# Kernel tuning notes

Hardware: AMD Instinct MI355X
Metric: run time of the kernel (lower is better)

## Reference

```python
import jax, jax.numpy as jnp
import numpy as np

N = 4096          # n_nodes
D = 7             # ligand_dim
H = 8             # dim_h
CUTOFF = 3.6      # bond_cutoff


def _linear_init(key, fan_in, fan_out):
    k1, k2 = jax.random.split(key)
    s = 1.0 / np.sqrt(fan_in)
    w = jax.random.uniform(k1, (fan_in, fan_out), minval=-s, maxval=s, dtype=jnp.float32)
    b = jax.random.uniform(k2, (fan_out,), minval=-s, maxval=s, dtype=jnp.float32)
    return w, b


def setup_inputs() -> dict:
    key = jax.random.key(0)
    ks = jax.random.split(key, 6)
    w1, b1 = _linear_init(ks[0], D, H)          # model layer 1
    w2, b2 = _linear_init(ks[1], H, H)          # model layer 2
    w3, b3 = _linear_init(ks[2], H, D + 16)     # model layer 3 (feats | keys | queries)
    we, be = _linear_init(ks[3], 2 * D, H)      # encoder
    wd, bd = _linear_init(ks[4], H, D)          # decoder
    x = jax.random.normal(ks[5], (N, D), dtype=jnp.float32)
    return dict(x=x, w1=w1, b1=b1, w2=w2, b2=b2, w3=w3, b3=b3,
                we=we, be=be, wd=wd, bd=bd)


def reference(x, w1, b1, w2, b2, w3, b3, we, be, wd, bd):
    # --- build_graph on detached x: L1 distance over first 3 coords ---
    # (sum(sqrt(abs(a-b)**2)) == sum(abs(a-b)))
    pos = jax.lax.stop_gradient(x[:, :3])
    dist = jnp.zeros((N, N), dtype=x.dtype)
    for d in range(3):  # loop over 3 coords to avoid an [N,N,3] intermediate
        dist = dist + jnp.abs(pos[:, d][:, None] - pos[None, :, d])
    A = (dist <= CUTOFF).astype(x.dtype)  # [N, N] adjacency
    # temp_input[-1] is never reset in the original kk loop, so node kk's
    # attention list is the cumulative multiset of neighbors of nodes 0..kk.
    C = jnp.cumsum(A, axis=0)             # [N, N] multiplicity of node l in kk's list

    # --- tiny MLP (shared per node) ---
    h = jnp.arctan(x @ w1 + b1)
    h = jnp.arctan(h @ w2 + b2)
    m = h @ w3 + b3                       # [N, D+16]
    feats = m[:, :D]                      # aggregated message payload
    keys_ = m[:, D:D + 8]                 # temp[:, -16:-8]
    queries = m[:, D + 8:]                # temp[:, -8:]

    # attention score of a list element depends only on its source node:
    # score = dot(queries[mm], keys[mm])
    s = jnp.sum(queries * keys_, axis=1)  # [N]

    # softmax over the cumulative multiset: weight of node l in row kk is
    # C[kk,l] * exp(s_l) / sum_l' C[kk,l'] * exp(s_l')   (stable via masked max)
    mask = C > 0
    smax = jnp.max(jnp.where(mask, s[None, :], -jnp.inf), axis=1)    # [N]
    w = C * jnp.where(mask, jnp.exp(s[None, :] - smax[:, None]), 0.0)  # [N, N]
    agg = (w @ feats) / jnp.sum(w, axis=1, keepdims=True)            # [N, D]

    # --- encode / decode ---
    codes = jnp.arctan(jnp.concatenate([x, agg], axis=1) @ we + be)  # [N, H]
    new_graph = codes @ wd + bd                                      # [N, D]
    return new_graph
```

## Files before the change

### kernel.cpp

```cpp
#include <hip/hip_runtime.h>
#include <math.h>

#define NN 4096
#define DD 7
#define HH 8
#define CUT 3.6f
#define JSPLIT 16
#define JCH 256
#define NRT 16
#define TPB 512


__global__ __launch_bounds__(TPB) void k_pair(
    const float* __restrict__ x,
    const float* __restrict__ w1, const float* __restrict__ b1,
    const float* __restrict__ w2, const float* __restrict__ b2,
    const float* __restrict__ w3, const float* __restrict__ b3,
    float* __restrict__ part, float* __restrict__ bsum)
{
    __shared__ float4 tile[JCH * 3];
    __shared__ float  red1[64][8];
    __shared__ float  red2[8][8];
    const int xb = blockIdx.x;
    const int y  = blockIdx.y;
    const int t  = threadIdx.x;

    if (t < JCH) {
        const int jg = y * JCH + t;
        float xi[DD];
#pragma unroll
        for (int i = 0; i < DD; ++i) xi[i] = x[jg * DD + i];

        float h1[HH];
#pragma unroll
        for (int o = 0; o < HH; ++o) {
            float a = b1[o];
#pragma unroll
            for (int i = 0; i < DD; ++i) a = fmaf(xi[i], w1[i * HH + o], a);
            h1[o] = atanf(a);
        }
        float h2[HH];
#pragma unroll
        for (int o = 0; o < HH; ++o) {
            float a = b2[o];
#pragma unroll
            for (int i = 0; i < HH; ++i) a = fmaf(h1[i], w2[i * HH + o], a);
            h2[o] = atanf(a);
        }
        float m[23];
#pragma unroll
        for (int c = 0; c < 23; ++c) {
            float a = b3[c];
#pragma unroll
            for (int i = 0; i < HH; ++i) a = fmaf(h2[i], w3[i * 23 + c], a);
            m[c] = a;
        }
        float s = 0.f;
#pragma unroll
        for (int k = 0; k < 8; ++k) s = fmaf(m[15 + k], m[7 + k], s);
        const float e = expf(s);

        tile[t * 3 + 0] = make_float4(xi[0], xi[1], xi[2], e);
        tile[t * 3 + 1] = make_float4(e * m[0], e * m[1], e * m[2], e * m[3]);
        tile[t * 3 + 2] = make_float4(e * m[4], e * m[5], e * m[6], 0.f);
    }
    __syncthreads();

    const int jl   = t & 7;
    const int grp  = t >> 3;
    const int row0 = xb * 256 + grp * 4;

    float px[4][3];
#pragma unroll
    for (int rr = 0; rr < 4; ++rr) {
        px[rr][0] = x[(row0 + rr) * DD + 0];
        px[rr][1] = x[(row0 + rr) * DD + 1];
        px[rr][2] = x[(row0 + rr) * DD + 2];
    }

    float acc[4][8];
#pragma unroll
    for (int rr = 0; rr < 4; ++rr)
#pragma unroll
        for (int ch = 0; ch < 8; ++ch) acc[rr][ch] = 0.f;

#pragma unroll 4
    for (int k = 0; k < JCH / 8; ++k) {
        const int jj = k * 8 + jl;
        float4 a = tile[jj * 3 + 0];
        float4 b = tile[jj * 3 + 1];
        float4 c = tile[jj * 3 + 2];
#pragma unroll
        for (int rr = 0; rr < 4; ++rr) {
            float dist = fabsf(px[rr][0] - a.x) + fabsf(px[rr][1] - a.y)
                       + fabsf(px[rr][2] - a.z);
            float msel = (dist <= CUT) ? 1.0f : 0.0f;
            acc[rr][0] = fmaf(msel, b.x, acc[rr][0]);
            acc[rr][1] = fmaf(msel, b.y, acc[rr][1]);
            acc[rr][2] = fmaf(msel, b.z, acc[rr][2]);
            acc[rr][3] = fmaf(msel, b.w, acc[rr][3]);
            acc[rr][4] = fmaf(msel, c.x, acc[rr][4]);
            acc[rr][5] = fmaf(msel, c.y, acc[rr][5]);
            acc[rr][6] = fmaf(msel, c.z, acc[rr][6]);
            acc[rr][7] = fmaf(msel, a.w, acc[rr][7]);
        }
    }

#pragma unroll
    for (int rr = 0; rr < 4; ++rr)
#pragma unroll
        for (int ch = 0; ch < 8; ++ch) {
            float v = acc[rr][ch];
            v += __shfl_xor(v, 4, 8);
            v += __shfl_xor(v, 2, 8);
            v += __shfl_xor(v, 1, 8);
            acc[rr][ch] = v;
        }

    if (jl == 0) {
#pragma unroll
        for (int ch = 0; ch < 8; ++ch) {
            float4* pp = (float4*)(part + (size_t)(y * 8 + ch) * NN + row0);
            *pp = make_float4(acc[0][ch], acc[1][ch], acc[2][ch], acc[3][ch]);
            red1[grp][ch] = ((acc[0][ch] + acc[1][ch]) + (acc[2][ch] + acc[3][ch]));
        }
    }
    __syncthreads();
    if (t < 64) {
        const int ch = t & 7, seg = t >> 3;
        float s = 0.f;
#pragma unroll
        for (int g = 0; g < 8; ++g) s += red1[seg * 8 + g][ch];
        red2[seg][ch] = s;
    }
    __syncthreads();
    if (t < 8) {
        float s = 0.f;
#pragma unroll
        for (int seg = 0; seg < 8; ++seg) s += red2[seg][t];
        bsum[xb * 128 + y * 8 + t] = s;
    }
}

__global__ __launch_bounds__(256) void k_scanfinal(
    const float* __restrict__ x, const float* __restrict__ part,
    const float* __restrict__ bsum,
    const float* __restrict__ we, const float* __restrict__ be,
    const float* __restrict__ wd, const float* __restrict__ bd,
    float* __restrict__ out)
{
    const int b = blockIdx.x;
    const int t = threadIdx.x;

    __shared__ float red[256];
    __shared__ float basech[8];
    __shared__ float wtot[4][8];

    {
        float p = 0.f;
        for (int i = t; i < b * 128; i += 256) p += bsum[i];
        red[t] = p;
    }
    __syncthreads();
    if (t < 8) {
        float s = 0.f;
#pragma unroll
        for (int q = 0; q < 32; ++q) s += red[t + 8 * q];
        basech[t] = s;
    }

    const int k = b * 256 + t;
    float T[8];
#pragma unroll
    for (int ch = 0; ch < 8; ++ch) {
        float v = 0.f;
#pragma unroll
        for (int y = 0; y < JSPLIT; ++y)
            v += part[(size_t)(y * 8 + ch) * NN + k];
        T[ch] = v;
    }

    const int lane = t & 63, wv = t >> 6;
    float sc[8];
#pragma unroll
    for (int ch = 0; ch < 8; ++ch) {
        float v = T[ch];
#pragma unroll
        for (int off = 1; off < 64; off <<= 1) {
            float o = __shfl_up(v, off, 64);
            if (lane >= off) v += o;
        }
        if (lane == 63) wtot[wv][ch] = v;
        sc[ch] = v;
    }
    __syncthreads();

    float pref[8];
#pragma unroll
    for (int ch = 0; ch < 8; ++ch) {
        float woff = basech[ch];
#pragma unroll
        for (int w = 0; w < 4; ++w) if (w < wv) woff += wtot[w][ch];
        pref[ch] = woff + sc[ch];
    }

    float v[14];
#pragma unroll
    for (int i = 0; i < DD; ++i) v[i] = x[k * DD + i];
    const float den = pref[7];
#pragma unroll
    for (int d = 0; d < DD; ++d) v[DD + d] = pref[d] / den;

    float codes[HH];
#pragma unroll
    for (int o = 0; o < HH; ++o) {
        float a = be[o];
#pragma unroll
        for (int i = 0; i < 14; ++i) a = fmaf(v[i], we[i * HH + o], a);
        codes[o] = atanf(a);
    }
#pragma unroll
    for (int d = 0; d < DD; ++d) {
        float a = bd[d];
#pragma unroll
        for (int o = 0; o < HH; ++o) a = fmaf(codes[o], wd[o * DD + d], a);
        out[k * DD + d] = a;
    }
}

extern "C" void kernel_launch(void* const* d_in, const int* in_sizes, int n_in,
                              void* d_out, int out_size, void* d_ws, size_t ws_size,
                              hipStream_t stream)
{
    const float* x  = (const float*)d_in[0];
    const float* w1 = (const float*)d_in[1];
    const float* b1 = (const float*)d_in[2];
    const float* w2 = (const float*)d_in[3];
    const float* b2 = (const float*)d_in[4];
    const float* w3 = (const float*)d_in[5];
    const float* b3 = (const float*)d_in[6];
    const float* we = (const float*)d_in[7];
    const float* be = (const float*)d_in[8];
    const float* wd = (const float*)d_in[9];
    const float* bd = (const float*)d_in[10];
    float* out = (float*)d_out;

    float* part = (float*)d_ws;
    float* bsum = part + (size_t)JSPLIT * 8 * NN;

    k_pair     <<<dim3(NRT, JSPLIT), TPB, 0, stream>>>(x, w1, b1, w2, b2, w3, b3,
                                                       part, bsum);
    k_scanfinal<<<NRT, 256, 0, stream>>>(x, part, bsum, we, be, wd, bd, out);
}
```

Before: 26.22 us.

## Fuse pair and scan kernels using a global atomic grid barrier

Merges the pairwise accumulation kernel and the scan/finalize kernel into one launch. All 256 blocks bump a global counter when done, and the first 16 blocks spin on it before running the prefix scan and the encoder/decoder. This removes the gap between dependent kernel launches, but adds a memset launch to reset the counter, busy-waiting, and the assumption that every block is resident at once. It also places a __syncthreads inside a branch only half the threads take.

```diff
diff --git a/kernel.cpp b/kernel.cpp
--- a/kernel.cpp
+++ b/kernel.cpp
@@ -9,21 +9,30 @@
 #define JCH 256
 #define NRT 16
 #define TPB 512
-
-
-__global__ __launch_bounds__(TPB) void k_pair(
+#define NBLK (NRT * JSPLIT)
+
+
+__global__ __launch_bounds__(TPB) void k_fused(
     const float* __restrict__ x,
     const float* __restrict__ w1, const float* __restrict__ b1,
     const float* __restrict__ w2, const float* __restrict__ b2,
     const float* __restrict__ w3, const float* __restrict__ b3,
-    float* __restrict__ part, float* __restrict__ bsum)
+    const float* __restrict__ we, const float* __restrict__ be,
+    const float* __restrict__ wd, const float* __restrict__ bd,
+    float* __restrict__ part, float* __restrict__ bsum,
+    int* __restrict__ sem, float* __restrict__ out)
 {
     __shared__ float4 tile[JCH * 3];
     __shared__ float  red1[64][8];
     __shared__ float  red2[8][8];
-    const int xb = blockIdx.x;
-    const int y  = blockIdx.y;
-    const int t  = threadIdx.x;
+    __shared__ float  red[256];
+    __shared__ float  basech[8];
+    __shared__ float  wtot[4][8];
+
+    const int blk = blockIdx.x;
+    const int xb  = blk >> 4;
+    const int y   = blk & 15;
+    const int t   = threadIdx.x;
 
     if (t < JCH) {
         const int jg = y * JCH + t;
@@ -140,23 +149,22 @@
         for (int seg = 0; seg < 8; ++seg) s += red2[seg][t];
         bsum[xb * 128 + y * 8 + t] = s;
     }
-}
-
-__global__ __launch_bounds__(256) void k_scanfinal(
-    const float* __restrict__ x, const float* __restrict__ part,
-    const float* __restrict__ bsum,
-    const float* __restrict__ we, const float* __restrict__ be,
-    const float* __restrict__ wd, const float* __restrict__ bd,
-    float* __restrict__ out)
-{
-    const int b = blockIdx.x;
-    const int t = threadIdx.x;
-
-    __shared__ float red[256];
-    __shared__ float basech[8];
-    __shared__ float wtot[4][8];
-
-    {
+
+    __threadfence();
+    __syncthreads();
+    if (t == 0)
+        __hip_atomic_fetch_add(sem, 1, __ATOMIC_RELEASE, __HIP_MEMORY_SCOPE_AGENT);
+    if (blk >= 16) return;
+
+    if (t == 0) {
+        while (__hip_atomic_load(sem, __ATOMIC_ACQUIRE, __HIP_MEMORY_SCOPE_AGENT)
+               < NBLK) {}
+    }
+    __syncthreads();
+    __threadfence();
+
+    const int b = blk;
+    if (t < 256) {
         float p = 0.f;
         for (int i = t; i < b * 128; i += 256) p += bsum[i];
         red[t] = p;
@@ -168,63 +176,66 @@
         for (int q = 0; q < 32; ++q) s += red[t + 8 * q];
         basech[t] = s;
     }
-
-    const int k = b * 256 + t;
-    float T[8];
-#pragma unroll
-    for (int ch = 0; ch < 8; ++ch) {
-        float v = 0.f;
-#pragma unroll
-        for (int y = 0; y < JSPLIT; ++y)
-            v += part[(size_t)(y * 8 + ch) * NN + k];
-        T[ch] = v;
-    }
-
-    const int lane = t & 63, wv = t >> 6;
-    float sc[8];
-#pragma unroll
-    for (int ch = 0; ch < 8; ++ch) {
-        float v = T[ch];
-#pragma unroll
-        for (int off = 1; off < 64; off <<= 1) {
-            float o = __shfl_up(v, off, 64);
-            if (lane >= off) v += o;
-        }
-        if (lane == 63) wtot[wv][ch] = v;
-        sc[ch] = v;
-    }
-    __syncthreads();
-
-    float pref[8];
-#pragma unroll
-    for (int ch = 0; ch < 8; ++ch) {
-        float woff = basech[ch];
-#pragma unroll
-        for (int w = 0; w < 4; ++w) if (w < wv) woff += wtot[w][ch];
-        pref[ch] = woff + sc[ch];
-    }
-
-    float v[14];
-#pragma unroll
-    for (int i = 0; i < DD; ++i) v[i] = x[k * DD + i];
-    const float den = pref[7];
-#pragma unroll
-    for (int d = 0; d < DD; ++d) v[DD + d] = pref[d] / den;
-
-    float codes[HH];
-#pragma unroll
-    for (int o = 0; o < HH; ++o) {
-        float a = be[o];
-#pragma unroll
-        for (int i = 0; i < 14; ++i) a = fmaf(v[i], we[i * HH + o], a);
-        codes[o] = atanf(a);
-    }
-#pragma unroll
-    for (int d = 0; d < DD; ++d) {
-        float a = bd[d];
-#pragma unroll
-        for (int o = 0; o < HH; ++o) a = fmaf(codes[o], wd[o * DD + d], a);
-        out[k * DD + d] = a;
+    __syncthreads();
+
+    if (t < 256) {
+        const int k = b * 256 + t;
+        float T[8];
+#pragma unroll
+        for (int ch = 0; ch < 8; ++ch) {
+            float v = 0.f;
+#pragma unroll
+            for (int yy = 0; yy < JSPLIT; ++yy)
+                v += part[(size_t)(yy * 8 + ch) * NN + k];
+            T[ch] = v;
+        }
+
+        const int lane = t & 63, wv = t >> 6;
+        float sc[8];
+#pragma unroll
+        for (int ch = 0; ch < 8; ++ch) {
+            float v = T[ch];
+#pragma unroll
+            for (int off = 1; off < 64; off <<= 1) {
+                float o = __shfl_up(v, off, 64);
+                if (lane >= off) v += o;
+            }
+            if (lane == 63) wtot[wv][ch] = v;
+            sc[ch] = v;
+        }
+        __syncthreads();
+
+        float pref[8];
+#pragma unroll
+        for (int ch = 0; ch < 8; ++ch) {
+            float woff = basech[ch];
+#pragma unroll
+            for (int w = 0; w < 4; ++w) if (w < wv) woff += wtot[w][ch];
+            pref[ch] = woff + sc[ch];
+        }
+
+        float v[14];
+#pragma unroll
+        for (int i = 0; i < DD; ++i) v[i] = x[k * DD + i];
+        const float den = pref[7];
+#pragma unroll
+        for (int d = 0; d < DD; ++d) v[DD + d] = pref[d] / den;
+
+        float codes[HH];
+#pragma unroll
+        for (int o = 0; o < HH; ++o) {
+            float a = be[o];
+#pragma unroll
+            for (int i = 0; i < 14; ++i) a = fmaf(v[i], we[i * HH + o], a);
+            codes[o] = atanf(a);
+        }
+#pragma unroll
+        for (int d = 0; d < DD; ++d) {
+            float a = bd[d];
+#pragma unroll
+            for (int o = 0; o < HH; ++o) a = fmaf(codes[o], wd[o * DD + d], a);
+            out[k * DD + d] = a;
+        }
     }
 }
 
@@ -247,8 +258,9 @@
 
     float* part = (float*)d_ws;
     float* bsum = part + (size_t)JSPLIT * 8 * NN;
-
-    k_pair     <<<dim3(NRT, JSPLIT), TPB, 0, stream>>>(x, w1, b1, w2, b2, w3, b3,
-                                                       part, bsum);
-    k_scanfinal<<<NRT, 256, 0, stream>>>(x, part, bsum, we, be, wd, bd, out);
+    int*   sem  = (int*)(bsum + NRT * JSPLIT * 8);
+
+    hipMemsetAsync((void*)sem, 0, sizeof(int), stream);
+    k_fused<<<NBLK, TPB, 0, stream>>>(x, w1, b1, w2, b2, w3, b3,
+                                      we, be, wd, bd, part, bsum, sem, out);
 }
```

New measurement: 71.33 us. +172.0%, slower.
